# Kernel optimization log

Hardware: AMD Instinct MI355X
Metric: run time of the kernel (lower is better)

## Reference

```python
import jax, jax.numpy as jnp
import numpy as np
from functools import partial

NUM_STEPS = 30  # Euler integration steps (inte_steps)


def _point_sample(vol, pts):
    """Trilinear sample of vol [C,D,H,W] at pts [N,3] (voxel coords, (d,h,w) order).
    Matches torch grid_sample(mode='bilinear', padding_mode='border', align_corners=True)
    after the normalize+flip done in PointPooling. Returns [C,N]."""
    dims = jnp.asarray(vol.shape[1:], dtype=pts.dtype)  # (D,H,W)
    p = jnp.clip(pts, 0.0, dims - 1.0)  # border padding == clamp coords
    p0 = jnp.floor(p)
    frac = p - p0  # [N,3]
    i0 = p0.astype(jnp.int32)
    i1 = jnp.minimum(i0 + 1, (dims - 1.0).astype(jnp.int32))
    d0, h0, w0 = i0[:, 0], i0[:, 1], i0[:, 2]
    d1, h1, w1 = i1[:, 0], i1[:, 1], i1[:, 2]
    fd, fh, fw = frac[:, 0], frac[:, 1], frac[:, 2]
    g = lambda d, h, w: vol[:, d, h, w]  # [C,N] gather
    c000, c001 = g(d0, h0, w0), g(d0, h0, w1)
    c010, c011 = g(d0, h1, w0), g(d0, h1, w1)
    c100, c101 = g(d1, h0, w0), g(d1, h0, w1)
    c110, c111 = g(d1, h1, w0), g(d1, h1, w1)
    c00 = c000 * (1 - fw) + c001 * fw
    c01 = c010 * (1 - fw) + c011 * fw
    c10 = c100 * (1 - fw) + c101 * fw
    c11 = c110 * (1 - fw) + c111 * fw
    c0 = c00 * (1 - fh) + c01 * fh
    c1 = c10 * (1 - fh) + c11 * fh
    return c0 * (1 - fd) + c1 * fd  # [C,N]


def _interp(flow, x):
    # flow [B,3,D,H,W], x [B,N,3] -> [B,N,3]
    out = jax.vmap(_point_sample)(flow, x)  # [B,3,N]
    return jnp.transpose(out, (0, 2, 1))


def _integrate_euler(flow, x, num_steps):
    flow = flow * (1.0 / num_steps)
    def step(x, _):
        return x + _interp(flow, x), None
    x, _ = jax.lax.scan(step, x, None, length=num_steps)
    return x


def _forward(verts, affine, flow_field):
    B, N, _ = verts.shape
    ones = jnp.ones((B, N, 1), dtype=verts.dtype)
    homog = jnp.concatenate([verts, ones], axis=-1)  # [B,N,4]
    pred = jnp.einsum('bij,bnj->bni', affine, homog)[..., :3]
    aux = _integrate_euler(flow_field, pred, NUM_STEPS)
    flow_int = aux - pred  # [B,N,3]
    pred = aux
    flow_int = jnp.transpose(flow_int, (0, 2, 1))[..., None, None]  # [B,3,N,1,1]
    homog2 = jnp.concatenate([pred, ones], axis=-1)
    inv_aff = jnp.linalg.inv(affine)
    pred = jnp.einsum('bij,bnj->bni', inv_aff, homog2)[..., :3]
    return pred, flow_int


def setup_inputs() -> dict:
    key = jax.random.key(0)
    k1, k2, k3 = jax.random.split(key, 3)
    B, N = 2, 140000
    D = H = W = 192
    dims = jnp.asarray([D - 1, H - 1, W - 1], dtype=jnp.float32)
    verts = jax.random.uniform(k1, (B, N, 3), dtype=jnp.float32) * dims
    affine = jnp.eye(4, dtype=jnp.float32)[None] + 0.01 * jax.random.normal(k2, (B, 4, 4), dtype=jnp.float32)
    flow_field = jax.random.normal(k3, (B, 3, D, H, W), dtype=jnp.float32)
    return {"verts": verts, "affine": affine, "flow_field": flow_field}


def reference(verts, affine, flow_field):
    return _forward(verts, affine, flow_field)
```

## Files before the change

### kernel.cpp

```cpp
#include <hip/hip_runtime.h>
#include <hip/hip_fp16.h>

#define NSTEPS 30
#define DIM 192
static constexpr long DHW = (long)DIM * DIM * DIM;
static constexpr int PTS_PER_WAVE = 21;

__global__ void invert4x4_kernel(const float* __restrict__ aff,
                                 float* __restrict__ out, int B) {
    int b = blockIdx.x * blockDim.x + threadIdx.x;
    if (b >= B) return;
    double a[16];
#pragma unroll
    for (int i = 0; i < 16; i++) a[i] = (double)aff[b * 16 + i];
    double s0 = a[0]*a[5]  - a[4]*a[1];
    double s1 = a[0]*a[6]  - a[4]*a[2];
    double s2 = a[0]*a[7]  - a[4]*a[3];
    double s3 = a[1]*a[6]  - a[5]*a[2];
    double s4 = a[1]*a[7]  - a[5]*a[3];
    double s5 = a[2]*a[7]  - a[6]*a[3];
    double c5 = a[10]*a[15] - a[14]*a[11];
    double c4 = a[9]*a[15]  - a[13]*a[11];
    double c3 = a[9]*a[14]  - a[13]*a[10];
    double c2 = a[8]*a[15]  - a[12]*a[11];
    double c1 = a[8]*a[14]  - a[12]*a[10];
    double c0 = a[8]*a[13]  - a[12]*a[9];
    double det = s0*c5 - s1*c4 + s2*c3 + s3*c2 - s4*c1 + s5*c0;
    double inv = 1.0 / det;
    double o[16];
    o[0]  = ( a[5]*c5 - a[6]*c4 + a[7]*c3) * inv;
    o[1]  = (-a[1]*c5 + a[2]*c4 - a[3]*c3) * inv;
    o[2]  = ( a[13]*s5 - a[14]*s4 + a[15]*s3) * inv;
    o[3]  = (-a[9]*s5 + a[10]*s4 - a[11]*s3) * inv;
    o[4]  = (-a[4]*c5 + a[6]*c2 - a[7]*c1) * inv;
    o[5]  = ( a[0]*c5 - a[2]*c2 + a[3]*c1) * inv;
    o[6]  = (-a[12]*s5 + a[14]*s2 - a[15]*s1) * inv;
    o[7]  = ( a[8]*s5 - a[10]*s2 + a[11]*s1) * inv;
    o[8]  = ( a[4]*c4 - a[5]*c2 + a[7]*c0) * inv;
    o[9]  = (-a[0]*c4 + a[1]*c2 - a[3]*c0) * inv;
    o[10] = ( a[12]*s4 - a[13]*s2 + a[15]*s0) * inv;
    o[11] = (-a[8]*s4 + a[9]*s2 - a[11]*s0) * inv;
    o[12] = (-a[4]*c3 + a[5]*c1 - a[6]*c0) * inv;
    o[13] = ( a[0]*c3 - a[1]*c1 + a[2]*c0) * inv;
    o[14] = (-a[12]*s3 + a[13]*s1 - a[14]*s0) * inv;
    o[15] = ( a[8]*s3 - a[9]*s1 + a[10]*s0) * inv;
#pragma unroll
    for (int i = 0; i < 16; i++) out[b * 16 + i] = (float)o[i];
}

__global__ __launch_bounds__(256) void repack4_kernel(const float* __restrict__ flow,
                                                      __half* __restrict__ packed) {
    long q = (long)blockIdx.x * blockDim.x + threadIdx.x;
    int b = blockIdx.y;
    long v0 = q * 4;
    if (v0 >= DHW) return;
    const float* F = flow + (size_t)b * 3 * DHW;
    float4 f0 = *reinterpret_cast<const float4*>(F + v0);
    float4 f1 = *reinterpret_cast<const float4*>(F + v0 + DHW);
    float4 f2 = *reinterpret_cast<const float4*>(F + v0 + 2 * DHW);
    union { __half2 h[2]; int2 i2; } u;
    int4 o0, o1;
    u.h[0] = __floats2half2_rn(f0.x, f1.x); u.h[1] = __floats2half2_rn(f2.x, 0.f);
    o0.x = u.i2.x; o0.y = u.i2.y;
    u.h[0] = __floats2half2_rn(f0.y, f1.y); u.h[1] = __floats2half2_rn(f2.y, 0.f);
    o0.z = u.i2.x; o0.w = u.i2.y;
    u.h[0] = __floats2half2_rn(f0.z, f1.z); u.h[1] = __floats2half2_rn(f2.z, 0.f);
    o1.x = u.i2.x; o1.y = u.i2.y;
    u.h[0] = __floats2half2_rn(f0.w, f1.w); u.h[1] = __floats2half2_rn(f2.w, 0.f);
    o1.z = u.i2.x; o1.w = u.i2.y;
    int4* out = reinterpret_cast<int4*>(packed) + (((size_t)b * DHW + v0) >> 1);
    out[0] = o0;
    out[1] = o1;
}

static __device__ __forceinline__ float2 h2f(unsigned u) {
    return __half22float2(__builtin_bit_cast(__half2, u));
}

__global__ __launch_bounds__(256) void deform4_kernel(
    const float* __restrict__ verts,
    const float* __restrict__ affine,
    const __half* __restrict__ packed,
    const float* __restrict__ invaff,
    float* __restrict__ out_pred,
    float* __restrict__ out_flow,
    int N, int B) {
    long t = (long)blockIdx.x * blockDim.x + threadIdx.x;
    long total = (long)B * N;
    long pt = t >> 2;
    int sub = (int)(t & 3);
    bool valid = pt < total;
    long i = valid ? pt : total - 1;
    int b = (int)(i / N);
    int n = (int)(i - (long)b * N);
    int hsel = sub & 1;
    int dsel = (sub >> 1) & 1;

    const float* A = affine + b * 16;
    const float* v = verts + (size_t)i * 3;
    float vx = v[0], vy = v[1], vz = v[2];
    float x = A[0] * vx + A[1] * vy + A[2]  * vz + A[3];
    float y = A[4] * vx + A[5] * vy + A[6]  * vz + A[7];
    float z = A[8] * vx + A[9] * vy + A[10] * vz + A[11];
    const float px = x, py = y, pz = z;

    const char* Pb = (const char*)(packed + (size_t)b * DHW * 4);
    const float scale = (float)(1.0 / NSTEPS);

    float cw0[3], cw1[3];
    int key = -1;

    for (int s = 0; s < NSTEPS; s++) {
        float pd = fminf(fmaxf(x, 0.0f), (float)(DIM - 1));
        float ph = fminf(fmaxf(y, 0.0f), (float)(DIM - 1));
        float pw = fminf(fmaxf(z, 0.0f), (float)(DIM - 1));
        float fd0 = floorf(pd), fh0 = floorf(ph), fw0 = floorf(pw);
        int d0 = (int)fd0, h0 = (int)fh0, w0 = (int)fw0;
        float fd = pd - fd0, fh = ph - fh0, fw = pw - fw0;

        int k = (d0 * DIM + h0) * DIM + w0;
        if (k != key) {
            key = k;
            int d1 = min(d0 + 1, DIM - 1);
            int h1 = min(h0 + 1, DIM - 1);
            int dr = dsel ? d1 : d0;
            int hr = hsel ? h1 : h0;
            int lb = min(w0, DIM - 2);
            int sel = w0 - lb;
            const uint2* p = reinterpret_cast<const uint2*>(
                Pb + (size_t)((dr * DIM + hr) * DIM + lb) * 8);
            uint2 qa = p[0];
            uint2 qb = p[1];
            float2 a01 = h2f(qa.x), a2_ = h2f(qa.y);
            float2 b01 = h2f(qb.x), b2_ = h2f(qb.y);
            cw0[0] = (sel ? b01.x : a01.x) * scale;
            cw0[1] = (sel ? b01.y : a01.y) * scale;
            cw0[2] = (sel ? b2_.x : a2_.x) * scale;
            cw1[0] = b01.x * scale;
            cw1[1] = b01.y * scale;
            cw1[2] = b2_.x * scale;
        }

        float omfw = 1.0f - fw;
        float wgt = (hsel ? fh : 1.0f - fh) * (dsel ? fd : 1.0f - fd);
        float v0 = (cw0[0] * omfw + cw1[0] * fw) * wgt;
        float v1 = (cw0[1] * omfw + cw1[1] * fw) * wgt;
        float v2 = (cw0[2] * omfw + cw1[2] * fw) * wgt;
        v0 += __shfl_xor(v0, 1, 64); v0 += __shfl_xor(v0, 2, 64);
        v1 += __shfl_xor(v1, 1, 64); v1 += __shfl_xor(v1, 2, 64);
        v2 += __shfl_xor(v2, 1, 64); v2 += __shfl_xor(v2, 2, 64);
        x += v0; y += v1; z += v2;
    }

    if (valid && sub < 3) {
        float posc = (sub == 0) ? x : (sub == 1) ? y : z;
        float p0c  = (sub == 0) ? px : (sub == 1) ? py : pz;
        float fint = posc - p0c;
        const float* Ai = invaff + b * 16 + sub * 4;
        float o = Ai[0] * x + Ai[1] * y + Ai[2] * z + Ai[3];
        out_pred[(size_t)i * 3 + sub] = o;
        out_flow[(size_t)b * 3 * N + (size_t)sub * N + n] = fint;
    }
}

__global__ __launch_bounds__(256) void deform_kernel(
    const float* __restrict__ verts,
    const float* __restrict__ affine,
    const float* __restrict__ flow,
    const float* __restrict__ invaff,
    float* __restrict__ out_pred,
    float* __restrict__ out_flow,
    int N, int B) {
    int lane = threadIdx.x & 63;
    int wib  = threadIdx.x >> 6;
    long gwave = (long)blockIdx.x * (blockDim.x >> 6) + wib;
    int piw = lane / 3;
    if (piw > PTS_PER_WAVE - 1) piw = PTS_PER_WAVE - 1;
    int ch = lane - piw * 3;
    if (ch > 2) ch = 2;
    long pt = gwave * PTS_PER_WAVE + piw;
    bool valid = (lane < 63) && (pt < (long)B * N);
    long ptc = valid ? pt : ((long)B * N - 1);
    int b = (int)(ptc / N);
    int n = (int)(ptc - (long)b * N);
    const float* A = affine + b * 16;
    const float* v = verts + (size_t)ptc * 3;
    float vx = v[0], vy = v[1], vz = v[2];
    float x = A[0] * vx + A[1] * vy + A[2]  * vz + A[3];
    float y = A[4] * vx + A[5] * vy + A[6]  * vz + A[7];
    float z = A[8] * vx + A[9] * vy + A[10] * vz + A[11];
    float p0 = (ch == 0) ? x : (ch == 1) ? y : z;
    const float* Fc = flow + ((size_t)b * 3 + ch) * (size_t)DHW;
    const float scale = (float)(1.0 / NSTEPS);
    float cc[8];
    int key = -1;
    int bl = piw * 3;
    for (int s = 0; s < NSTEPS; s++) {
        float pd = fminf(fmaxf(x, 0.0f), (float)(DIM - 1));
        float ph = fminf(fmaxf(y, 0.0f), (float)(DIM - 1));
        float pw = fminf(fmaxf(z, 0.0f), (float)(DIM - 1));
        float fd0 = floorf(pd), fh0 = floorf(ph), fw0 = floorf(pw);
        int d0 = (int)fd0, h0 = (int)fh0, w0 = (int)fw0;
        float fd = pd - fd0, fh = ph - fh0, fw = pw - fw0;
        int k = (d0 * DIM + h0) * DIM + w0;
        if (k != key) {
            key = k;
            int d1 = min(d0 + 1, DIM - 1);
            int h1 = min(h0 + 1, DIM - 1);
            int w1 = min(w0 + 1, DIM - 1);
            int r00 = (d0 * DIM + h0) * DIM;
            int r01 = (d0 * DIM + h1) * DIM;
            int r10 = (d1 * DIM + h0) * DIM;
            int r11 = (d1 * DIM + h1) * DIM;
            cc[0] = Fc[r00 + w0] * scale;
            cc[1] = Fc[r00 + w1] * scale;
            cc[2] = Fc[r01 + w0] * scale;
            cc[3] = Fc[r01 + w1] * scale;
            cc[4] = Fc[r10 + w0] * scale;
            cc[5] = Fc[r10 + w1] * scale;
            cc[6] = Fc[r11 + w0] * scale;
            cc[7] = Fc[r11 + w1] * scale;
        }
        float omfw = 1.0f - fw, omfh = 1.0f - fh, omfd = 1.0f - fd;
        float c00 = cc[0] * omfw + cc[1] * fw;
        float c01 = cc[2] * omfw + cc[3] * fw;
        float c10 = cc[4] * omfw + cc[5] * fw;
        float c11 = cc[6] * omfw + cc[7] * fw;
        float c0 = c00 * omfh + c01 * fh;
        float c1 = c10 * omfh + c11 * fh;
        float val = c0 * omfd + c1 * fd;
        float v0 = __shfl(val, bl,     64);
        float v1 = __shfl(val, bl + 1, 64);
        float v2 = __shfl(val, bl + 2, 64);
        x += v0; y += v1; z += v2;
    }
    if (valid) {
        float posc = (ch == 0) ? x : (ch == 1) ? y : z;
        float fint = posc - p0;
        const float* Ai = invaff + b * 16 + ch * 4;
        float o = Ai[0] * x + Ai[1] * y + Ai[2] * z + Ai[3];
        out_pred[(size_t)ptc * 3 + ch] = o;
        out_flow[(size_t)b * 3 * N + (size_t)ch * N + n] = fint;
    }
}

extern "C" void kernel_launch(void* const* d_in, const int* in_sizes, int n_in,
                              void* d_out, int out_size, void* d_ws, size_t ws_size,
                              hipStream_t stream) {
    const float* verts  = (const float*)d_in[0];
    const float* affine = (const float*)d_in[1];
    const float* flow   = (const float*)d_in[2];

    int B = in_sizes[1] / 16;
    int N = in_sizes[0] / (3 * B);

    float* out_pred = (float*)d_out;
    float* out_flow = out_pred + (size_t)B * N * 3;

    size_t packed_bytes = (size_t)B * DHW * 4 * sizeof(__half);
    bool use_packed = (ws_size >= packed_bytes + 256);

    long total = (long)B * N;

    if (use_packed) {
        __half* packed = (__half*)d_ws;
        float* invaff  = (float*)((char*)d_ws + packed_bytes);
        hipLaunchKernelGGL(invert4x4_kernel, dim3(1), dim3(64), 0, stream,
                           affine, invaff, B);
        long quads = (DHW + 3) / 4;
        long vblocks = (quads + 255) / 256;
        hipLaunchKernelGGL(repack4_kernel, dim3((unsigned)vblocks, B), dim3(256), 0,
                           stream, flow, packed);
        long threads = total * 4;
        long blocks = (threads + 255) / 256;
        hipLaunchKernelGGL(deform4_kernel, dim3((unsigned)blocks), dim3(256), 0,
                           stream, verts, affine, packed, invaff,
                           out_pred, out_flow, N, B);
    } else {
        float* invaff = (float*)d_ws;
        hipLaunchKernelGGL(invert4x4_kernel, dim3(1), dim3(64), 0, stream,
                           affine, invaff, B);
        long waves  = (total + PTS_PER_WAVE - 1) / PTS_PER_WAVE;
        long blocks = (waves + 3) / 4;
        hipLaunchKernelGGL(deform_kernel, dim3((unsigned)blocks), dim3(256), 0,
                           stream, verts, affine, flow, invaff,
                           out_pred, out_flow, N, B);
    }
}
```

Baseline: 315.6 us.

## Use eight lanes per point, one trilinear corner each, prescale flow in repack

The deform kernel now assigns eight lanes per point instead of four. Each lane fetches a single 8-byte corner and the weighted sum is reduced with three xor shuffles, where previously each lane loaded two w-neighbours. The 1/NSTEPS scale is folded into the fp16 repack, removing a multiply in the inner loop. This doubles the thread count and adds one more shuffle level per step, in exchange for lower per-lane work and fewer registers.

```diff
diff --git a/kernel.cpp b/kernel.cpp
--- a/kernel.cpp
+++ b/kernel.cpp
@@ -54,19 +54,20 @@
     int b = blockIdx.y;
     long v0 = q * 4;
     if (v0 >= DHW) return;
+    const float s = (float)(1.0 / NSTEPS);
     const float* F = flow + (size_t)b * 3 * DHW;
     float4 f0 = *reinterpret_cast<const float4*>(F + v0);
     float4 f1 = *reinterpret_cast<const float4*>(F + v0 + DHW);
     float4 f2 = *reinterpret_cast<const float4*>(F + v0 + 2 * DHW);
     union { __half2 h[2]; int2 i2; } u;
     int4 o0, o1;
-    u.h[0] = __floats2half2_rn(f0.x, f1.x); u.h[1] = __floats2half2_rn(f2.x, 0.f);
+    u.h[0] = __floats2half2_rn(f0.x*s, f1.x*s); u.h[1] = __floats2half2_rn(f2.x*s, 0.f);
     o0.x = u.i2.x; o0.y = u.i2.y;
-    u.h[0] = __floats2half2_rn(f0.y, f1.y); u.h[1] = __floats2half2_rn(f2.y, 0.f);
+    u.h[0] = __floats2half2_rn(f0.y*s, f1.y*s); u.h[1] = __floats2half2_rn(f2.y*s, 0.f);
     o0.z = u.i2.x; o0.w = u.i2.y;
-    u.h[0] = __floats2half2_rn(f0.z, f1.z); u.h[1] = __floats2half2_rn(f2.z, 0.f);
+    u.h[0] = __floats2half2_rn(f0.z*s, f1.z*s); u.h[1] = __floats2half2_rn(f2.z*s, 0.f);
     o1.x = u.i2.x; o1.y = u.i2.y;
-    u.h[0] = __floats2half2_rn(f0.w, f1.w); u.h[1] = __floats2half2_rn(f2.w, 0.f);
+    u.h[0] = __floats2half2_rn(f0.w*s, f1.w*s); u.h[1] = __floats2half2_rn(f2.w*s, 0.f);
     o1.z = u.i2.x; o1.w = u.i2.y;
     int4* out = reinterpret_cast<int4*>(packed) + (((size_t)b * DHW + v0) >> 1);
     out[0] = o0;
@@ -77,7 +78,7 @@
     return __half22float2(__builtin_bit_cast(__half2, u));
 }
 
-__global__ __launch_bounds__(256) void deform4_kernel(
+__global__ __launch_bounds__(256) void deform8_kernel(
     const float* __restrict__ verts,
     const float* __restrict__ affine,
     const __half* __restrict__ packed,
@@ -87,14 +88,15 @@
     int N, int B) {
     long t = (long)blockIdx.x * blockDim.x + threadIdx.x;
     long total = (long)B * N;
-    long pt = t >> 2;
-    int sub = (int)(t & 3);
+    long pt = t >> 3;
+    int sub = (int)(t & 7);
     bool valid = pt < total;
     long i = valid ? pt : total - 1;
     int b = (int)(i / N);
     int n = (int)(i - (long)b * N);
-    int hsel = sub & 1;
-    int dsel = (sub >> 1) & 1;
+    int wsel = sub & 1;
+    int hsel = (sub >> 1) & 1;
+    int dsel = (sub >> 2) & 1;
 
     const float* A = affine + b * 16;
     const float* v = verts + (size_t)i * 3;
@@ -105,9 +107,8 @@
     const float px = x, py = y, pz = z;
 
     const char* Pb = (const char*)(packed + (size_t)b * DHW * 4);
-    const float scale = (float)(1.0 / NSTEPS);
-
-    float cw0[3], cw1[3];
+
+    float c0 = 0.f, c1 = 0.f, c2 = 0.f;
     int key = -1;
 
     for (int s = 0; s < NSTEPS; s++) {
@@ -121,34 +122,23 @@
         int k = (d0 * DIM + h0) * DIM + w0;
         if (k != key) {
             key = k;
-            int d1 = min(d0 + 1, DIM - 1);
-            int h1 = min(h0 + 1, DIM - 1);
-            int dr = dsel ? d1 : d0;
-            int hr = hsel ? h1 : h0;
-            int lb = min(w0, DIM - 2);
-            int sel = w0 - lb;
-            const uint2* p = reinterpret_cast<const uint2*>(
-                Pb + (size_t)((dr * DIM + hr) * DIM + lb) * 8);
-            uint2 qa = p[0];
-            uint2 qb = p[1];
-            float2 a01 = h2f(qa.x), a2_ = h2f(qa.y);
-            float2 b01 = h2f(qb.x), b2_ = h2f(qb.y);
-            cw0[0] = (sel ? b01.x : a01.x) * scale;
-            cw0[1] = (sel ? b01.y : a01.y) * scale;
-            cw0[2] = (sel ? b2_.x : a2_.x) * scale;
-            cw1[0] = b01.x * scale;
-            cw1[1] = b01.y * scale;
-            cw1[2] = b2_.x * scale;
+            int dr = dsel ? min(d0 + 1, DIM - 1) : d0;
+            int hr = hsel ? min(h0 + 1, DIM - 1) : h0;
+            int wr = wsel ? min(w0 + 1, DIM - 1) : w0;
+            uint2 q = *reinterpret_cast<const uint2*>(
+                Pb + (size_t)((dr * DIM + hr) * DIM + wr) * 8);
+            float2 q01 = h2f(q.x), q2_ = h2f(q.y);
+            c0 = q01.x; c1 = q01.y; c2 = q2_.x;
         }
 
-        float omfw = 1.0f - fw;
-        float wgt = (hsel ? fh : 1.0f - fh) * (dsel ? fd : 1.0f - fd);
-        float v0 = (cw0[0] * omfw + cw1[0] * fw) * wgt;
-        float v1 = (cw0[1] * omfw + cw1[1] * fw) * wgt;
-        float v2 = (cw0[2] * omfw + cw1[2] * fw) * wgt;
-        v0 += __shfl_xor(v0, 1, 64); v0 += __shfl_xor(v0, 2, 64);
-        v1 += __shfl_xor(v1, 1, 64); v1 += __shfl_xor(v1, 2, 64);
-        v2 += __shfl_xor(v2, 1, 64); v2 += __shfl_xor(v2, 2, 64);
+        float ww = wsel ? fw : 1.0f - fw;
+        float wh = hsel ? fh : 1.0f - fh;
+        float wd = dsel ? fd : 1.0f - fd;
+        float w = ww * wh * wd;
+        float v0 = c0 * w, v1 = c1 * w, v2 = c2 * w;
+        v0 += __shfl_xor(v0, 1, 64); v0 += __shfl_xor(v0, 2, 64); v0 += __shfl_xor(v0, 4, 64);
+        v1 += __shfl_xor(v1, 1, 64); v1 += __shfl_xor(v1, 2, 64); v1 += __shfl_xor(v1, 4, 64);
+        v2 += __shfl_xor(v2, 1, 64); v2 += __shfl_xor(v2, 2, 64); v2 += __shfl_xor(v2, 4, 64);
         x += v0; y += v1; z += v2;
     }
 
@@ -253,14 +243,13 @@
 
     int B = in_sizes[1] / 16;
     int N = in_sizes[0] / (3 * B);
+    long total = (long)B * N;
 
     float* out_pred = (float*)d_out;
     float* out_flow = out_pred + (size_t)B * N * 3;
 
     size_t packed_bytes = (size_t)B * DHW * 4 * sizeof(__half);
     bool use_packed = (ws_size >= packed_bytes + 256);
-
-    long total = (long)B * N;
 
     if (use_packed) {
         __half* packed = (__half*)d_ws;
@@ -271,9 +260,9 @@
         long vblocks = (quads + 255) / 256;
         hipLaunchKernelGGL(repack4_kernel, dim3((unsigned)vblocks, B), dim3(256), 0,
                            stream, flow, packed);
-        long threads = total * 4;
+        long threads = total * 8;
         long blocks = (threads + 255) / 256;
-        hipLaunchKernelGGL(deform4_kernel, dim3((unsigned)blocks), dim3(256), 0,
+        hipLaunchKernelGGL(deform8_kernel, dim3((unsigned)blocks), dim3(256), 0,
                            stream, verts, affine, packed, invaff,
                            out_pred, out_flow, N, B);
     } else {
```

After: 366.0 us. 16.0% more time.
